# Kernel optimization log

Hardware: AMD Instinct MI355X
Metric: run time of the kernel (lower is better)

The kernel has to match this reference:

```python
import jax, jax.numpy as jnp
import numpy as np

TEMPERATURE = 0.1
EPS_NORM = 1e-12  # torch F.normalize eps
EPS_LOSS = 1e-8


def setup_inputs() -> dict:
    key = jax.random.key(0)
    k1, k2 = jax.random.split(key)
    N, D, K = 8192, 512, 64
    features = jax.random.normal(k1, (N, D), dtype=jnp.float32)
    cluster_assignments = jax.random.randint(k2, (N,), 0, K, dtype=jnp.int64)
    return {"features": features, "cluster_assignments": cluster_assignments}


def reference(features, cluster_assignments):
    # L2 normalize rows (torch.nn.functional.normalize, p=2, dim=1)
    norm = jnp.linalg.norm(features, axis=1, keepdims=True)
    features_norm = features / jnp.maximum(norm, EPS_NORM)
    # pairwise cosine similarity scaled by temperature -> [N, N]
    sim = jnp.einsum('id,jd->ij', features_norm, features_norm) / TEMPERATURE
    exp_sim = jnp.exp(sim)
    mask = (cluster_assignments[None, :] == cluster_assignments[:, None]).astype(exp_sim.dtype)
    pos_sum = jnp.sum(exp_sim * mask, axis=1, keepdims=True)
    neg_sum = jnp.sum(exp_sim * (1.0 - mask), axis=1, keepdims=True)
    loss = -jnp.log(pos_sum / (pos_sum + neg_sum + EPS_LOSS))
    return jnp.sum(loss)  # reduction='sum'
```

## Files before the change

### kernel.cpp

```cpp
#include <hip/hip_runtime.h>
#include <hip/hip_bf16.h>
#include <stdint.h>

#define N 8192
#define D 512
#define TILE 128
#define BK 64
#define NKC (D / BK)
#define NTB (N / TILE)
#define NBLK (NTB * (NTB + 1) / 2)
#define PANEL_BYTES (TILE * D)
#define KCHUNK_BYTES (TILE * BK)

typedef long long i64;
typedef __attribute__((ext_vector_type(4))) float f32x4;

__device__ __forceinline__ void gload_lds16(const void* gp, const void* lp) {
    auto g = (const __attribute__((address_space(1))) void*)(uintptr_t)gp;
    auto l = (__attribute__((address_space(3))) void*)(uintptr_t)lp;
    __builtin_amdgcn_global_load_lds(g, l, 16, 0, 0);
}


__global__ void cc_normalize(const float* __restrict__ F, uint8_t* __restrict__ Fn2,
                             float* __restrict__ out) {
    if (blockIdx.x == 0 && threadIdx.x == 0) out[0] = 0.0f;
    const int row  = blockIdx.x * 4 + (threadIdx.x >> 6);
    const int lane = threadIdx.x & 63;
    const float* p = F + (size_t)row * D + lane * 8;
    float4 a = *(const float4*)p;
    float4 b = *(const float4*)(p + 4);
    float ss = a.x*a.x + a.y*a.y + a.z*a.z + a.w*a.w
             + b.x*b.x + b.y*b.y + b.z*b.z + b.w*b.w;
    #pragma unroll
    for (int m = 32; m; m >>= 1) ss += __shfl_xor(ss, m, 64);
    const float inv = 16.0f / fmaxf(sqrtf(ss), 1e-12f);
    int lo = 0, hi = 0;
    lo = __builtin_amdgcn_cvt_pk_fp8_f32(a.x*inv, a.y*inv, lo, false);
    lo = __builtin_amdgcn_cvt_pk_fp8_f32(a.z*inv, a.w*inv, lo, true);
    hi = __builtin_amdgcn_cvt_pk_fp8_f32(b.x*inv, b.y*inv, hi, false);
    hi = __builtin_amdgcn_cvt_pk_fp8_f32(b.z*inv, b.w*inv, hi, true);
    const size_t idx = (size_t)(row >> 7) * PANEL_BYTES + (size_t)lane * 1024 + (row & 127) * 8;
    *(int2*)(Fn2 + idx) = make_int2(lo, hi);
}

__global__ __launch_bounds__(256, 4)
void cc_gemm(const uint8_t* __restrict__ Fn2, const int* __restrict__ cl,
             float* __restrict__ Pt, float* __restrict__ Pp) {
    __shared__ __align__(16) uint8_t As[2][KCHUNK_BYTES];
    __shared__ __align__(16) uint8_t Bs[2][KCHUNK_BYTES];
    __shared__ int crow[TILE], ccol[TILE];
    __shared__ float rsum[2][TILE][2];
    __shared__ float csum[2][TILE][2];

    const int tid  = threadIdx.x;
    const int wave = tid >> 6;
    const int lane = tid & 63;

    int rem = blockIdx.x, bm = 0;
    while (rem >= NTB - bm) { rem -= NTB - bm; ++bm; }
    const int bn = bm + rem;
    const bool diag = (bm == bn);

    if (tid < TILE)            crow[tid]        = cl[bm * TILE + tid];
    else                       ccol[tid - TILE] = cl[bn * TILE + (tid - TILE)];

    const int wr = wave >> 1, wc = wave & 1;
    const int q   = lane >> 4;
    const int n15 = lane & 15;

    f32x4 acc[4][4];
    #pragma unroll
    for (int t = 0; t < 4; ++t)
        #pragma unroll
        for (int u = 0; u < 4; ++u) acc[t][u] = (f32x4)(0.0f);

    const uint8_t* Ag = Fn2 + (size_t)bm * PANEL_BYTES;
    const uint8_t* Bg = Fn2 + (size_t)bn * PANEL_BYTES;

    #pragma unroll
    for (int i = 0; i < 2; ++i) {
        const int off = (wave * 2 + i) * 1024;
        gload_lds16(Ag + off + lane * 16, &As[0][off]);
        gload_lds16(Bg + off + lane * 16, &Bs[0][off]);
    }

    for (int kc = 0; kc < NKC; ++kc) {
        const int b = kc & 1;
        __syncthreads();
        if (kc + 1 < NKC) {
            const uint8_t* ga = Ag + (kc + 1) * KCHUNK_BYTES;
            const uint8_t* gb = Bg + (kc + 1) * KCHUNK_BYTES;
            #pragma unroll
            for (int i = 0; i < 2; ++i) {
                const int off = (wave * 2 + i) * 1024;
                gload_lds16(ga + off + lane * 16, &As[b ^ 1][off]);
                gload_lds16(gb + off + lane * 16, &Bs[b ^ 1][off]);
            }
        }
        #pragma unroll
        for (int ks = 0; ks < 2; ++ks) {
            const int base = ks * 4096 + q * 1024 + n15 * 8;
            i64 af[4], bfr[4];
            #pragma unroll
            for (int t = 0; t < 4; ++t)
                af[t] = *(const i64*)&As[b][base + (wr * 64 + t * 16) * 8];
            #pragma unroll
            for (int u = 0; u < 4; ++u)
                bfr[u] = *(const i64*)&Bs[b][base + (wc * 64 + u * 16) * 8];
            #pragma unroll
            for (int t = 0; t < 4; ++t)
                #pragma unroll
                for (int u = 0; u < 4; ++u)
                    acc[t][u] = __builtin_amdgcn_mfma_f32_16x16x32_fp8_fp8(af[t], bfr[u], acc[t][u], 0, 0, 0);
        }
    }

    const float SC = 0.05635527503472514f;
    int cc[4];
    #pragma unroll
    for (int u = 0; u < 4; ++u) cc[u] = ccol[wc * 64 + u * 16 + n15];

    float ce[4] = {0.f, 0.f, 0.f, 0.f};
    float cp[4] = {0.f, 0.f, 0.f, 0.f};

    #pragma unroll
    for (int t = 0; t < 4; ++t) {
        #pragma unroll
        for (int r = 0; r < 4; ++r) {
            const int lr  = wr * 64 + t * 16 + q * 4 + r;
            const int myc = crow[lr];
            float te = 0.0f, tp = 0.0f;
            #pragma unroll
            for (int u = 0; u < 4; ++u) {
                const float e  = exp2f(acc[t][u][r] * SC);
                const float ep = (cc[u] == myc) ? e : 0.0f;
                te += e;  tp += ep;
                ce[u] += e;  cp[u] += ep;
            }
            #pragma unroll
            for (int m = 1; m < 16; m <<= 1) {
                te += __shfl_xor(te, m, 64);
                tp += __shfl_xor(tp, m, 64);
            }
            if (n15 == 0) { rsum[wc][lr][0] = te; rsum[wc][lr][1] = tp; }
        }
    }

    if (!diag) {
        #pragma unroll
        for (int u = 0; u < 4; ++u) {
            float e = ce[u], p = cp[u];
            e += __shfl_xor(e, 16, 64);  p += __shfl_xor(p, 16, 64);
            e += __shfl_xor(e, 32, 64);  p += __shfl_xor(p, 32, 64);
            if (lane < 16) {
                const int lc = wc * 64 + u * 16 + n15;
                csum[wr][lc][0] = e;  csum[wr][lc][1] = p;
            }
        }
    }

    __syncthreads();
    if (tid < TILE) {
        const float te = rsum[0][tid][0] + rsum[1][tid][0];
        const float tp = rsum[0][tid][1] + rsum[1][tid][1];
        const size_t o = (size_t)bn * N + bm * TILE + tid;
        Pt[o] = te;  Pp[o] = tp;
    } else if (!diag) {
        const int c = tid - TILE;
        const float te = csum[0][c][0] + csum[1][c][0];
        const float tp = csum[0][c][1] + csum[1][c][1];
        const size_t o = (size_t)bm * N + bn * TILE + c;
        Pt[o] = te;  Pp[o] = tp;
    }
}

__global__ void cc_finalize(const float* __restrict__ Pt, const float* __restrict__ Pp,
                            float* __restrict__ out) {
    __shared__ float red[4];
    const int i = blockIdx.x * 256 + threadIdx.x;
    float tv = 0.0f, pv = 0.0f;
    #pragma unroll 8
    for (int s = 0; s < NTB; ++s) {
        tv += Pt[(size_t)s * N + i];
        pv += Pp[(size_t)s * N + i];
    }
    float l = __logf(tv + 1e-8f) - __logf(pv);
    #pragma unroll
    for (int m = 32; m; m >>= 1) l += __shfl_xor(l, m, 64);
    const int wv = threadIdx.x >> 6, lane = threadIdx.x & 63;
    if (lane == 0) red[wv] = l;
    __syncthreads();
    if (threadIdx.x == 0) atomicAdd(out, red[0] + red[1] + red[2] + red[3]);
}

extern "C" void kernel_launch(void* const* d_in, const int* in_sizes, int n_in,
                              void* d_out, int out_size, void* d_ws, size_t ws_size,
                              hipStream_t stream) {
    const float* F  = (const float*)d_in[0];
    const int*   cl = (const int*)d_in[1];
    float* out = (float*)d_out;

    uint8_t* Fn2 = (uint8_t*)d_ws;
    float* Pt  = (float*)((char*)d_ws + (size_t)N * D);
    float* Pp  = Pt + (size_t)NTB * N;

    cc_normalize<<<N / 4, 256, 0, stream>>>(F, Fn2, out);
    cc_gemm<<<NBLK, 256, 0, stream>>>(Fn2, cl, Pt, Pp);
    cc_finalize<<<N / 256, 256, 0, stream>>>(Pt, Pp, out);
}
```

Before: 128.3 us.

## Use 8-wave blocks and XCD-aware triangular tile mapping in similarity GEMM

The GEMM block grows from 4 to 8 waves arranged 4x2, so each wave computes a 32x64 sub-tile instead of 64x64. This halves per-wave accumulators and load work and is meant to improve latency hiding and occupancy. Blocks are also remapped so that each XCD handles paired triangular rows p and 63-p. That balances work and keeps the same A panels within one XCD's L2. In exchange, B fragments are read from LDS by more waves, and the column partial reduction now sums four wave-row contributions.

```diff
diff --git a/kernel.cpp b/kernel.cpp
--- a/kernel.cpp
+++ b/kernel.cpp
@@ -20,7 +20,6 @@
     auto l = (__attribute__((address_space(3))) void*)(uintptr_t)lp;
     __builtin_amdgcn_global_load_lds(g, l, 16, 0, 0);
 }
-
 
 __global__ void cc_normalize(const float* __restrict__ F, uint8_t* __restrict__ Fn2,
                              float* __restrict__ out) {
@@ -44,46 +43,46 @@
     *(int2*)(Fn2 + idx) = make_int2(lo, hi);
 }
 
-__global__ __launch_bounds__(256, 4)
+__global__ __launch_bounds__(512, 6)
 void cc_gemm(const uint8_t* __restrict__ Fn2, const int* __restrict__ cl,
              float* __restrict__ Pt, float* __restrict__ Pp) {
     __shared__ __align__(16) uint8_t As[2][KCHUNK_BYTES];
     __shared__ __align__(16) uint8_t Bs[2][KCHUNK_BYTES];
     __shared__ int crow[TILE], ccol[TILE];
     __shared__ float rsum[2][TILE][2];
-    __shared__ float csum[2][TILE][2];
+    __shared__ float csum[4][TILE][2];
 
     const int tid  = threadIdx.x;
     const int wave = tid >> 6;
     const int lane = tid & 63;
 
-    int rem = blockIdx.x, bm = 0;
-    while (rem >= NTB - bm) { rem -= NTB - bm; ++bm; }
-    const int bn = bm + rem;
+    const int xcd = blockIdx.x & 7;
+    const int s   = blockIdx.x >> 3;
+    const int p   = xcd * 4 + s / 65;
+    const int j   = s % 65;
+    int bm, bn;
+    if (j < NTB - p) { bm = p;          bn = p + j; }
+    else             { bm = NTB - 1 - p; bn = bm + (j - (NTB - p)); }
     const bool diag = (bm == bn);
 
-    if (tid < TILE)            crow[tid]        = cl[bm * TILE + tid];
-    else                       ccol[tid - TILE] = cl[bn * TILE + (tid - TILE)];
+    if (tid < TILE)                         crow[tid]        = cl[bm * TILE + tid];
+    else if (tid < 2 * TILE)                ccol[tid - TILE] = cl[bn * TILE + (tid - TILE)];
 
     const int wr = wave >> 1, wc = wave & 1;
     const int q   = lane >> 4;
     const int n15 = lane & 15;
 
-    f32x4 acc[4][4];
-    #pragma unroll
-    for (int t = 0; t < 4; ++t)
+    f32x4 acc[2][4];
+    #pragma unroll
+    for (int t = 0; t < 2; ++t)
         #pragma unroll
         for (int u = 0; u < 4; ++u) acc[t][u] = (f32x4)(0.0f);
 
     const uint8_t* Ag = Fn2 + (size_t)bm * PANEL_BYTES;
     const uint8_t* Bg = Fn2 + (size_t)bn * PANEL_BYTES;
 
-    #pragma unroll
-    for (int i = 0; i < 2; ++i) {
-        const int off = (wave * 2 + i) * 1024;
-        gload_lds16(Ag + off + lane * 16, &As[0][off]);
-        gload_lds16(Bg + off + lane * 16, &Bs[0][off]);
-    }
+    gload_lds16(Ag + wave * 1024 + lane * 16, &As[0][wave * 1024]);
+    gload_lds16(Bg + wave * 1024 + lane * 16, &Bs[0][wave * 1024]);
 
     for (int kc = 0; kc < NKC; ++kc) {
         const int b = kc & 1;
@@ -91,25 +90,21 @@
         if (kc + 1 < NKC) {
             const uint8_t* ga = Ag + (kc + 1) * KCHUNK_BYTES;
             const uint8_t* gb = Bg + (kc + 1) * KCHUNK_BYTES;
-            #pragma unroll
-            for (int i = 0; i < 2; ++i) {
-                const int off = (wave * 2 + i) * 1024;
-                gload_lds16(ga + off + lane * 16, &As[b ^ 1][off]);
-                gload_lds16(gb + off + lane * 16, &Bs[b ^ 1][off]);
-            }
+            gload_lds16(ga + wave * 1024 + lane * 16, &As[b ^ 1][wave * 1024]);
+            gload_lds16(gb + wave * 1024 + lane * 16, &Bs[b ^ 1][wave * 1024]);
         }
         #pragma unroll
         for (int ks = 0; ks < 2; ++ks) {
             const int base = ks * 4096 + q * 1024 + n15 * 8;
-            i64 af[4], bfr[4];
-            #pragma unroll
-            for (int t = 0; t < 4; ++t)
-                af[t] = *(const i64*)&As[b][base + (wr * 64 + t * 16) * 8];
+            i64 af[2], bfr[4];
+            #pragma unroll
+            for (int t = 0; t < 2; ++t)
+                af[t] = *(const i64*)&As[b][base + (wr * 32 + t * 16) * 8];
             #pragma unroll
             for (int u = 0; u < 4; ++u)
                 bfr[u] = *(const i64*)&Bs[b][base + (wc * 64 + u * 16) * 8];
             #pragma unroll
-            for (int t = 0; t < 4; ++t)
+            for (int t = 0; t < 2; ++t)
                 #pragma unroll
                 for (int u = 0; u < 4; ++u)
                     acc[t][u] = __builtin_amdgcn_mfma_f32_16x16x32_fp8_fp8(af[t], bfr[u], acc[t][u], 0, 0, 0);
@@ -125,10 +120,10 @@
     float cp[4] = {0.f, 0.f, 0.f, 0.f};
 
     #pragma unroll
-    for (int t = 0; t < 4; ++t) {
+    for (int t = 0; t < 2; ++t) {
         #pragma unroll
         for (int r = 0; r < 4; ++r) {
-            const int lr  = wr * 64 + t * 16 + q * 4 + r;
+            const int lr  = wr * 32 + t * 16 + q * 4 + r;
             const int myc = crow[lr];
             float te = 0.0f, tp = 0.0f;
             #pragma unroll
@@ -150,12 +145,12 @@
     if (!diag) {
         #pragma unroll
         for (int u = 0; u < 4; ++u) {
-            float e = ce[u], p = cp[u];
-            e += __shfl_xor(e, 16, 64);  p += __shfl_xor(p, 16, 64);
-            e += __shfl_xor(e, 32, 64);  p += __shfl_xor(p, 32, 64);
+            float e = ce[u], p2 = cp[u];
+            e += __shfl_xor(e, 16, 64);  p2 += __shfl_xor(p2, 16, 64);
+            e += __shfl_xor(e, 32, 64);  p2 += __shfl_xor(p2, 32, 64);
             if (lane < 16) {
                 const int lc = wc * 64 + u * 16 + n15;
-                csum[wr][lc][0] = e;  csum[wr][lc][1] = p;
+                csum[wr][lc][0] = e;  csum[wr][lc][1] = p2;
             }
         }
     }
@@ -166,10 +161,10 @@
         const float tp = rsum[0][tid][1] + rsum[1][tid][1];
         const size_t o = (size_t)bn * N + bm * TILE + tid;
         Pt[o] = te;  Pp[o] = tp;
-    } else if (!diag) {
+    } else if (tid < 2 * TILE && !diag) {
         const int c = tid - TILE;
-        const float te = csum[0][c][0] + csum[1][c][0];
-        const float tp = csum[0][c][1] + csum[1][c][1];
+        const float te = csum[0][c][0] + csum[1][c][0] + csum[2][c][0] + csum[3][c][0];
+        const float tp = csum[0][c][1] + csum[1][c][1] + csum[2][c][1] + csum[3][c][1];
         const size_t o = (size_t)bm * N + bn * TILE + c;
         Pt[o] = te;  Pp[o] = tp;
     }
@@ -206,6 +201,6 @@
     float* Pp  = Pt + (size_t)NTB * N;
 
     cc_normalize<<<N / 4, 256, 0, stream>>>(F, Fn2, out);
-    cc_gemm<<<NBLK, 256, 0, stream>>>(Fn2, cl, Pt, Pp);
+    cc_gemm<<<NBLK, 512, 0, stream>>>(Fn2, cl, Pt, Pp);
     cc_finalize<<<N / 256, 256, 0, stream>>>(Pt, Pp, out);
 }
```

New measurement: 133.1 us. +3.7%, slower.

## Load GEMM fragments directly from global memory instead of LDS double buffering

Applied to the files above, without the earlier changes.

Removes the LDS staging buffers and async global-to-LDS double-buffered pipeline, and has each wave read its fp8 MFMA operand fragments directly from global memory (L1/L2) in an unrolled k-loop. The aim is to drop the per-chunk barriers and LDS traffic, and to raise occupancy by freeing shared memory. The cost is duplicate global reads across waves that share A/B rows, plus exposed global-load latency without an explicit prefetch stage.

```diff
diff --git a/kernel.cpp b/kernel.cpp
--- a/kernel.cpp
+++ b/kernel.cpp
@@ -5,22 +5,12 @@
 #define N 8192
 #define D 512
 #define TILE 128
-#define BK 64
-#define NKC (D / BK)
 #define NTB (N / TILE)
 #define NBLK (NTB * (NTB + 1) / 2)
 #define PANEL_BYTES (TILE * D)
-#define KCHUNK_BYTES (TILE * BK)
 
 typedef long long i64;
 typedef __attribute__((ext_vector_type(4))) float f32x4;
-
-__device__ __forceinline__ void gload_lds16(const void* gp, const void* lp) {
-    auto g = (const __attribute__((address_space(1))) void*)(uintptr_t)gp;
-    auto l = (__attribute__((address_space(3))) void*)(uintptr_t)lp;
-    __builtin_amdgcn_global_load_lds(g, l, 16, 0, 0);
-}
-
 
 __global__ void cc_normalize(const float* __restrict__ F, uint8_t* __restrict__ Fn2,
                              float* __restrict__ out) {
@@ -47,8 +37,6 @@
 __global__ __launch_bounds__(256, 4)
 void cc_gemm(const uint8_t* __restrict__ Fn2, const int* __restrict__ cl,
              float* __restrict__ Pt, float* __restrict__ Pp) {
-    __shared__ __align__(16) uint8_t As[2][KCHUNK_BYTES];
-    __shared__ __align__(16) uint8_t Bs[2][KCHUNK_BYTES];
     __shared__ int crow[TILE], ccol[TILE];
     __shared__ float rsum[2][TILE][2];
     __shared__ float csum[2][TILE][2];
@@ -75,45 +63,31 @@
         #pragma unroll
         for (int u = 0; u < 4; ++u) acc[t][u] = (f32x4)(0.0f);
 
-    const uint8_t* Ag = Fn2 + (size_t)bm * PANEL_BYTES;
-    const uint8_t* Bg = Fn2 + (size_t)bn * PANEL_BYTES;
+    const uint8_t* pa[4];
+    const uint8_t* pb[4];
+    #pragma unroll
+    for (int t = 0; t < 4; ++t)
+        pa[t] = Fn2 + (size_t)bm * PANEL_BYTES + q * 1024 + (wr * 64 + t * 16 + n15) * 8;
+    #pragma unroll
+    for (int u = 0; u < 4; ++u)
+        pb[u] = Fn2 + (size_t)bn * PANEL_BYTES + q * 1024 + (wc * 64 + u * 16 + n15) * 8;
 
-    #pragma unroll
-    for (int i = 0; i < 2; ++i) {
-        const int off = (wave * 2 + i) * 1024;
-        gload_lds16(Ag + off + lane * 16, &As[0][off]);
-        gload_lds16(Bg + off + lane * 16, &Bs[0][off]);
-    }
+    __syncthreads();
 
-    for (int kc = 0; kc < NKC; ++kc) {
-        const int b = kc & 1;
-        __syncthreads();
-        if (kc + 1 < NKC) {
-            const uint8_t* ga = Ag + (kc + 1) * KCHUNK_BYTES;
-            const uint8_t* gb = Bg + (kc + 1) * KCHUNK_BYTES;
-            #pragma unroll
-            for (int i = 0; i < 2; ++i) {
-                const int off = (wave * 2 + i) * 1024;
-                gload_lds16(ga + off + lane * 16, &As[b ^ 1][off]);
-                gload_lds16(gb + off + lane * 16, &Bs[b ^ 1][off]);
-            }
-        }
+    #pragma unroll 4
+    for (int kb = 0; kb < 16; ++kb) {
+        i64 af[4], bfr[4];
         #pragma unroll
-        for (int ks = 0; ks < 2; ++ks) {
-            const int base = ks * 4096 + q * 1024 + n15 * 8;
-            i64 af[4], bfr[4];
-            #pragma unroll
-            for (int t = 0; t < 4; ++t)
-                af[t] = *(const i64*)&As[b][base + (wr * 64 + t * 16) * 8];
+        for (int t = 0; t < 4; ++t)
+            af[t] = *(const i64*)(pa[t] + (size_t)kb * 4096);
+        #pragma unroll
+        for (int u = 0; u < 4; ++u)
+            bfr[u] = *(const i64*)(pb[u] + (size_t)kb * 4096);
+        #pragma unroll
+        for (int t = 0; t < 4; ++t)
             #pragma unroll
             for (int u = 0; u < 4; ++u)
-                bfr[u] = *(const i64*)&Bs[b][base + (wc * 64 + u * 16) * 8];
-            #pragma unroll
-            for (int t = 0; t < 4; ++t)
-                #pragma unroll
-                for (int u = 0; u < 4; ++u)
-                    acc[t][u] = __builtin_amdgcn_mfma_f32_16x16x32_fp8_fp8(af[t], bfr[u], acc[t][u], 0, 0, 0);
-        }
+                acc[t][u] = __builtin_amdgcn_mfma_f32_16x16x32_fp8_fp8(af[t], bfr[u], acc[t][u], 0, 0, 0);
     }
 
     const float SC = 0.05635527503472514f;
@@ -150,12 +124,12 @@
     if (!diag) {
         #pragma unroll
         for (int u = 0; u < 4; ++u) {
-            float e = ce[u], p = cp[u];
-            e += __shfl_xor(e, 16, 64);  p += __shfl_xor(p, 16, 64);
-            e += __shfl_xor(e, 32, 64);  p += __shfl_xor(p, 32, 64);
+            float e = ce[u], p2 = cp[u];
+            e += __shfl_xor(e, 16, 64);  p2 += __shfl_xor(p2, 16, 64);
+            e += __shfl_xor(e, 32, 64);  p2 += __shfl_xor(p2, 32, 64);
             if (lane < 16) {
                 const int lc = wc * 64 + u * 16 + n15;
-                csum[wr][lc][0] = e;  csum[wr][lc][1] = p;
+                csum[wr][lc][0] = e;  csum[wr][lc][1] = p2;
             }
         }
     }
```

After: 135.8 us. +5.8%, slower.

## Fuse finalize reduction into GEMM using per-tile completion counters

Applied to the files above, without the earlier changes.

Removes the separate finalize kernel. Each GEMM block now stores its packed row and column partial sums as one 64-bit atomic store and increments a per-tile counter. The last block to finish a tile row reduces the 64 partials, computes the log loss, and atomically adds it to the output. This saves a kernel launch and the round trip through two float arrays. The risks are relaxed-ordering visibility, since no explicit release/acquire fence is used, and extra tail work in the last-arriving blocks.

```diff
diff --git a/kernel.cpp b/kernel.cpp
--- a/kernel.cpp
+++ b/kernel.cpp
@@ -13,6 +13,7 @@
 #define KCHUNK_BYTES (TILE * BK)
 
 typedef long long i64;
+typedef unsigned long long u64;
 typedef __attribute__((ext_vector_type(4))) float f32x4;
 
 __device__ __forceinline__ void gload_lds16(const void* gp, const void* lp) {
@@ -21,10 +22,16 @@
     __builtin_amdgcn_global_load_lds(g, l, 16, 0, 0);
 }
 
+__device__ __forceinline__ u64 pack2(float a, float b) {
+    union { float2 f; u64 u; } v; v.f = make_float2(a, b); return v.u;
+}
 
 __global__ void cc_normalize(const float* __restrict__ F, uint8_t* __restrict__ Fn2,
-                             float* __restrict__ out) {
-    if (blockIdx.x == 0 && threadIdx.x == 0) out[0] = 0.0f;
+                             int* __restrict__ tcnt, float* __restrict__ out) {
+    if (blockIdx.x == 0) {
+        if (threadIdx.x == 0) out[0] = 0.0f;
+        if (threadIdx.x < NTB) tcnt[threadIdx.x] = 0;
+    }
     const int row  = blockIdx.x * 4 + (threadIdx.x >> 6);
     const int lane = threadIdx.x & 63;
     const float* p = F + (size_t)row * D + lane * 8;
@@ -46,12 +53,14 @@
 
 __global__ __launch_bounds__(256, 4)
 void cc_gemm(const uint8_t* __restrict__ Fn2, const int* __restrict__ cl,
-             float* __restrict__ Pt, float* __restrict__ Pp) {
+             u64* __restrict__ P8, int* __restrict__ tcnt, float* __restrict__ out) {
     __shared__ __align__(16) uint8_t As[2][KCHUNK_BYTES];
     __shared__ __align__(16) uint8_t Bs[2][KCHUNK_BYTES];
     __shared__ int crow[TILE], ccol[TILE];
     __shared__ float rsum[2][TILE][2];
     __shared__ float csum[2][TILE][2];
+    __shared__ float red[4];
+    __shared__ int fin0, fin1;
 
     const int tid  = threadIdx.x;
     const int wave = tid >> 6;
@@ -150,48 +159,70 @@
     if (!diag) {
         #pragma unroll
         for (int u = 0; u < 4; ++u) {
-            float e = ce[u], p = cp[u];
-            e += __shfl_xor(e, 16, 64);  p += __shfl_xor(p, 16, 64);
-            e += __shfl_xor(e, 32, 64);  p += __shfl_xor(p, 32, 64);
+            float e = ce[u], p2 = cp[u];
+            e += __shfl_xor(e, 16, 64);  p2 += __shfl_xor(p2, 16, 64);
+            e += __shfl_xor(e, 32, 64);  p2 += __shfl_xor(p2, 32, 64);
             if (lane < 16) {
                 const int lc = wc * 64 + u * 16 + n15;
-                csum[wr][lc][0] = e;  csum[wr][lc][1] = p;
+                csum[wr][lc][0] = e;  csum[wr][lc][1] = p2;
             }
         }
     }
 
     __syncthreads();
     if (tid < TILE) {
-        const float te = rsum[0][tid][0] + rsum[1][tid][0];
-        const float tp = rsum[0][tid][1] + rsum[1][tid][1];
-        const size_t o = (size_t)bn * N + bm * TILE + tid;
-        Pt[o] = te;  Pp[o] = tp;
+        const u64 v = pack2(rsum[0][tid][0] + rsum[1][tid][0],
+                            rsum[0][tid][1] + rsum[1][tid][1]);
+        __hip_atomic_store(&P8[(size_t)bn * N + bm * TILE + tid], v,
+                           __ATOMIC_RELAXED, __HIP_MEMORY_SCOPE_AGENT);
     } else if (!diag) {
         const int c = tid - TILE;
-        const float te = csum[0][c][0] + csum[1][c][0];
-        const float tp = csum[0][c][1] + csum[1][c][1];
-        const size_t o = (size_t)bm * N + bn * TILE + c;
-        Pt[o] = te;  Pp[o] = tp;
-    }
-}
-
-__global__ void cc_finalize(const float* __restrict__ Pt, const float* __restrict__ Pp,
-                            float* __restrict__ out) {
-    __shared__ float red[4];
-    const int i = blockIdx.x * 256 + threadIdx.x;
-    float tv = 0.0f, pv = 0.0f;
-    #pragma unroll 8
-    for (int s = 0; s < NTB; ++s) {
-        tv += Pt[(size_t)s * N + i];
-        pv += Pp[(size_t)s * N + i];
-    }
-    float l = __logf(tv + 1e-8f) - __logf(pv);
-    #pragma unroll
-    for (int m = 32; m; m >>= 1) l += __shfl_xor(l, m, 64);
-    const int wv = threadIdx.x >> 6, lane = threadIdx.x & 63;
-    if (lane == 0) red[wv] = l;
+        const u64 v = pack2(csum[0][c][0] + csum[1][c][0],
+                            csum[0][c][1] + csum[1][c][1]);
+        __hip_atomic_store(&P8[(size_t)bm * N + bn * TILE + c], v,
+                           __ATOMIC_RELAXED, __HIP_MEMORY_SCOPE_AGENT);
+    }
     __syncthreads();
-    if (threadIdx.x == 0) atomicAdd(out, red[0] + red[1] + red[2] + red[3]);
+
+    if (tid == 0) {
+        fin0 = (__hip_atomic_fetch_add(&tcnt[bm], 1, __ATOMIC_RELAXED,
+                                       __HIP_MEMORY_SCOPE_AGENT) == NTB - 1);
+        fin1 = diag ? 0
+             : (__hip_atomic_fetch_add(&tcnt[bn], 1, __ATOMIC_RELAXED,
+                                       __HIP_MEMORY_SCOPE_AGENT) == NTB - 1);
+    }
+    __syncthreads();
+
+    #pragma unroll
+    for (int pass = 0; pass < 2; ++pass) {
+        const bool doit = pass == 0 ? (fin0 != 0) : (fin1 != 0);
+        if (!doit) continue;
+        const int t = pass == 0 ? bm : bn;
+        const int j = tid & 127, h = tid >> 7;
+        float tv = 0.f, pv = 0.f;
+        const u64* base = P8 + (size_t)(h * 32) * N + t * TILE + j;
+        #pragma unroll 8
+        for (int s = 0; s < 32; ++s) {
+            union { u64 u; float2 f; } w;
+            w.u = __hip_atomic_load(base + (size_t)s * N,
+                                    __ATOMIC_RELAXED, __HIP_MEMORY_SCOPE_AGENT);
+            tv += w.f.x;  pv += w.f.y;
+        }
+        rsum[h][j][0] = tv;  rsum[h][j][1] = pv;
+        __syncthreads();
+        float l = 0.0f;
+        if (tid < TILE) {
+            const float T  = rsum[0][tid][0] + rsum[1][tid][0];
+            const float Pv = rsum[0][tid][1] + rsum[1][tid][1];
+            l = __logf(T + 1e-8f) - __logf(Pv);
+        }
+        #pragma unroll
+        for (int m = 32; m; m >>= 1) l += __shfl_xor(l, m, 64);
+        if (lane == 0) red[wave] = l;
+        __syncthreads();
+        if (tid == 0) atomicAdd(out, red[0] + red[1] + red[2] + red[3]);
+        __syncthreads();
+    }
 }
 
 extern "C" void kernel_launch(void* const* d_in, const int* in_sizes, int n_in,
@@ -202,10 +233,9 @@
     float* out = (float*)d_out;
 
     uint8_t* Fn2 = (uint8_t*)d_ws;
-    float* Pt  = (float*)((char*)d_ws + (size_t)N * D);
-    float* Pp  = Pt + (size_t)NTB * N;
-
-    cc_normalize<<<N / 4, 256, 0, stream>>>(F, Fn2, out);
-    cc_gemm<<<NBLK, 256, 0, stream>>>(Fn2, cl, Pt, Pp);
-    cc_finalize<<<N / 256, 256, 0, stream>>>(Pt, Pp, out);
-}
+    u64*   P8   = (u64*)((char*)d_ws + (size_t)N * D);
+    int*   tcnt = (int*)((char*)d_ws + (size_t)N * D + (size_t)NTB * N * 8);
+
+    cc_normalize<<<N / 4, 256, 0, stream>>>(F, Fn2, tcnt, out);
+    cc_gemm<<<NBLK, 256, 0, stream>>>(Fn2, cl, P8, tcnt, out);
+}
```

Measured after the change: 134.2 us. 4.6% more time.
